# Performance work log

Measured on AMD Instinct MI355X. Metric: run time of the kernel, lower is better.

Reference implementation:

```python
import jax, jax.numpy as jnp
import numpy as np

D_MODEL = 1024
H = 16
D_K = D_MODEL // H
NEG = -1e9


def setup_inputs() -> dict:
    key = jax.random.key(0)
    ks = jax.random.split(key, 8)
    B, S = 4, 2048
    q = jax.random.normal(ks[0], (B, S, D_MODEL), dtype=jnp.float32)
    k = jax.random.normal(ks[1], (B, S, D_MODEL), dtype=jnp.float32)
    v = jax.random.normal(ks[2], (B, S, D_MODEL), dtype=jnp.float32)
    mask = jax.random.randint(ks[3], (B, S), 0, 2, dtype=jnp.int32)
    scale = 1.0 / np.sqrt(D_MODEL)
    Wq = jax.random.normal(ks[4], (D_MODEL, D_MODEL), dtype=jnp.float32) * scale
    Wk = jax.random.normal(ks[5], (D_MODEL, D_MODEL), dtype=jnp.float32) * scale
    Wv = jax.random.normal(ks[6], (D_MODEL, D_MODEL), dtype=jnp.float32) * scale
    Wo = jax.random.normal(ks[7], (D_MODEL, D_MODEL), dtype=jnp.float32) * scale
    return {"q": q, "k": k, "v": v, "mask": mask,
            "Wq": Wq, "Wk": Wk, "Wv": Wv, "Wo": Wo}


def _split_heads(x):
    # [B,S,d_model] -> [B,H,S,d_k]
    B, S, _ = x.shape
    return x.reshape(B, S, H, D_K).transpose(0, 2, 1, 3)


def reference(q, k, v, mask, Wq, Wk, Wv, Wo):
    # Linear projections (torch Linear: x @ W.T, no bias)
    query = _split_heads(jnp.einsum('bsd,ed->bse', q, Wq))
    key_ = _split_heads(jnp.einsum('bsd,ed->bse', k, Wk))
    value = _split_heads(jnp.einsum('bsd,ed->bse', v, Wv))
    # scaled dot-product attention, manual path
    scores = jnp.einsum('bhqd,bhkd->bhqk', query, key_) / jnp.sqrt(
        jnp.asarray(D_K, dtype=query.dtype))
    m = (mask == 0)[:, None, None, :]  # [B,1,1,S]
    scores = jnp.where(m, jnp.asarray(NEG, dtype=scores.dtype), scores)
    attn = jax.nn.softmax(scores, axis=-1)
    mh = jnp.einsum('bhqk,bhkd->bhqd', attn, value)
    # merge heads -> [B,S,d_model]
    B = mh.shape[0]
    mh = mh.transpose(0, 2, 1, 3).reshape(B, -1, D_MODEL)
    return jnp.einsum('bsd,ed->bse', mh, Wo)
```

## Files before the change

### kernel.cpp

```cpp
#include <hip/hip_runtime.h>
#include <math.h>

typedef __attribute__((ext_vector_type(4))) float f32x4;
typedef __attribute__((ext_vector_type(8))) __bf16 bf16x8;
typedef __attribute__((ext_vector_type(2))) __bf16 bf16x2;

#ifndef __has_builtin
#define __has_builtin(x) 0
#endif

#if __has_builtin(__builtin_amdgcn_exp2f)
#define EXP2F(x) __builtin_amdgcn_exp2f(x)
#else
#define EXP2F(x) exp2f(x)
#endif

__device__ __forceinline__ ushort f2bf(float f) {
  return (ushort)((__float_as_uint(f) + 0x8000u) >> 16);
}

__device__ __forceinline__ uint pack_bf16(float a, float b) {
#if __has_builtin(__builtin_amdgcn_cvt_pk_bf16_f32)
  bf16x2 p = __builtin_amdgcn_cvt_pk_bf16_f32(a, b);
  return __builtin_bit_cast(uint, p);
#elif __has_builtin(__builtin_amdgcn_perm)
  uint au = __float_as_uint(a) + 0x8000u;
  uint bu = __float_as_uint(b) + 0x8000u;
  return __builtin_amdgcn_perm(bu, au, 0x07060302u);
#else
  return (uint)f2bf(a) | ((uint)f2bf(b) << 16);
#endif
}

__device__ __forceinline__ void async_cp16(const void* g, void* l) {
  __builtin_amdgcn_global_load_lds(
      (const __attribute__((address_space(1))) void*)g,
      (__attribute__((address_space(3))) void*)l, 16, 0, 0);
}


__global__ __launch_bounds__(256) void prep_kernel(
    const float* __restrict__ q, const float* __restrict__ k, const float* __restrict__ v,
    const float* __restrict__ Wq, const float* __restrict__ Wk, const float* __restrict__ Wv,
    const float* __restrict__ Wo, const int* __restrict__ mask,
    ushort* qb, ushort* kb, ushort* vb,
    ushort* wqb, ushort* wkb, ushort* wvb, ushort* wob,
    ushort* biasbf) {
  int b = blockIdx.x;
  int tid = threadIdx.x;
  if (b < 4096) {
    int j = b >> 10;
    const float* in = j == 0 ? Wq : (j == 1 ? Wk : (j == 2 ? Wv : Wo));
    ushort* out = j == 0 ? wqb : (j == 1 ? wkb : (j == 2 ? wvb : wob));
    int i = (b & 1023) * 256 + tid;
    float4 f = ((const float4*)in)[i];
    uint2 o;
    o.x = pack_bf16(f.x, f.y);
    o.y = pack_bf16(f.z, f.w);
    ((uint2*)out)[i] = o;
  } else if (b < 28672) {
    int bb = b - 4096;
    int j = bb >> 13;
    const float* in = j == 0 ? q : (j == 1 ? k : v);
    ushort* out = j == 0 ? qb : (j == 1 ? kb : vb);
    int i = (bb & 8191) * 256 + tid;
    float4 f = ((const float4*)in)[i];
    uint2 o;
    o.x = pack_bf16(f.x, f.y);
    o.y = pack_bf16(f.z, f.w);
    ((uint2*)out)[i] = o;
  } else {
    int i = (b - 28672) * 256 + tid;
    biasbf[i] = mask[i] ? (ushort)0 : (ushort)0xCE6E;
  }
}


__device__ __forceinline__ void gemm_body(const ushort* __restrict__ A,
                                          const ushort* __restrict__ W,
                                          void* __restrict__ Cout, int mode,
                                          int bm, int bn) {
  constexpr int N = 1024, K = 1024;
  constexpr int NT = K / 64;
  __shared__ ushort As[2][128 * 64];
  __shared__ ushort Bs[2][64 * 64];
  const int tid = threadIdx.x;
  const int w = tid >> 6, lane = tid & 63;
  const int g = lane >> 4, cc = lane & 15;
  const int wm = (w >> 1) * 64, wn = (w & 1) * 32;

  f32x4 acc[4][2];
#pragma unroll
  for (int i = 0; i < 4; ++i)
#pragma unroll
    for (int j = 0; j < 2; ++j) acc[i][j] = (f32x4)0.0f;

  auto stage = [&](int k0, int buf) {
#pragma unroll
    for (int j = 0; j < 4; ++j) {
      int cbase = w * 256 + j * 64;
      int cid = cbase + lane;
      int row = cid & 127, kb = cid >> 7;
      async_cp16(A + (size_t)(bm + row) * K + k0 + kb * 8, &As[buf][cbase * 8]);
    }
#pragma unroll
    for (int j = 0; j < 2; ++j) {
      int cbase = w * 128 + j * 64;
      int cid = cbase + lane;
      int row = cid & 63, kb = cid >> 6;
      async_cp16(W + (size_t)(bn + row) * K + k0 + kb * 8, &Bs[buf][cbase * 8]);
    }
  };

  auto compute = [&](int cur) {
#pragma unroll
    for (int ks = 0; ks < 2; ++ks) {
      bf16x8 af[4], bfr[2];
#pragma unroll
      for (int mi = 0; mi < 4; ++mi)
        af[mi] = *(const bf16x8*)&As[cur][((ks * 4 + g) * 128 + wm + mi * 16 + cc) * 8];
#pragma unroll
      for (int ni = 0; ni < 2; ++ni)
        bfr[ni] = *(const bf16x8*)&Bs[cur][((ks * 4 + g) * 64 + wn + ni * 16 + cc) * 8];
      __builtin_amdgcn_s_setprio(1);
#pragma unroll
      for (int mi = 0; mi < 4; ++mi)
#pragma unroll
        for (int ni = 0; ni < 2; ++ni)
          acc[mi][ni] =
              __builtin_amdgcn_mfma_f32_16x16x32_bf16(af[mi], bfr[ni], acc[mi][ni], 0, 0, 0);
      __builtin_amdgcn_s_setprio(0);
    }
  };

  stage(0, 0);
  stage(64, 1);
  for (int it = 0; it < NT - 1; ++it) {
    const int cur = it & 1;
    asm volatile("s_waitcnt vmcnt(6)" ::: "memory");
    __builtin_amdgcn_s_barrier();
    __builtin_amdgcn_sched_barrier(0);
    compute(cur);
    __builtin_amdgcn_sched_barrier(0);
    __builtin_amdgcn_s_barrier();
    __builtin_amdgcn_sched_barrier(0);
    if (it < NT - 2) stage((it + 2) * 64, cur);
  }
  asm volatile("s_waitcnt vmcnt(0)" ::: "memory");
  __builtin_amdgcn_s_barrier();
  __builtin_amdgcn_sched_barrier(0);
  compute((NT - 1) & 1);

  const float qsc = 0.18033688011112042f;
#pragma unroll
  for (int mi = 0; mi < 4; ++mi) {
#pragma unroll
    for (int ni = 0; ni < 2; ++ni) {
#pragma unroll
      for (int r = 0; r < 4; ++r) {
        int row = bm + wm + mi * 16 + g * 4 + r;
        int col = bn + wn + ni * 16 + cc;
        float val = acc[mi][ni][r];
        if (mode == 0) {
          ((ushort*)Cout)[(size_t)row * N + col] = f2bf(val);
        } else if (mode == 1) {
          ((float*)Cout)[(size_t)row * N + col] = val;
        } else if (mode == 3) {
          ((ushort*)Cout)[(size_t)row * N + col] = f2bf(val * qsc);
        } else {
          int b = row >> 11, s = row & 2047;
          int h = col >> 6, d = col & 63;
          ((ushort*)Cout)[(size_t)((b * 16 + h) * 64 + d) * 2048 + s] = f2bf(val);
        }
      }
    }
  }
}

__device__ __forceinline__ void swz_tile(int* bm, int* bn) {
  int l = blockIdx.x + (blockIdx.y << 4);
  int t = ((l & 7) << 7) + (l >> 3);
  *bn = (t & 15) * 64;
  *bm = (t >> 4) * 128;
}

__global__ __launch_bounds__(256) void qkv_gemm_kernel(const ushort* qb, const ushort* kb,
                                                       const ushort* vb, const ushort* wq,
                                                       const ushort* wk, const ushort* wv,
                                                       ushort* Qp, ushort* Kp, ushort* Vt) {
  int z = blockIdx.z;
  const ushort* A = z == 0 ? qb : (z == 1 ? kb : vb);
  const ushort* W = z == 0 ? wq : (z == 1 ? wk : wv);
  void* C = z == 0 ? (void*)Qp : (z == 1 ? (void*)Kp : (void*)Vt);
  int bm, bn;
  swz_tile(&bm, &bn);
  gemm_body(A, W, C, z == 2 ? 2 : (z == 0 ? 3 : 0), bm, bn);
}

__global__ __launch_bounds__(256) void gemm_wo_kernel(const ushort* A, const ushort* W,
                                                      float* C) {
  int bm, bn;
  swz_tile(&bm, &bn);
  gemm_body(A, W, C, 1, bm, bn);
}

__global__ __launch_bounds__(256, 3) void attn_kernel(const ushort* __restrict__ Qp,
                                                      const ushort* __restrict__ Kp,
                                                      const ushort* __restrict__ Vt,
                                                      const ushort* __restrict__ biasbf,
                                                      ushort* __restrict__ mh) {
  constexpr int S = 2048, DM = 1024, DK = 64;
  constexpr int NKT = S / 64;
  __shared__ ushort k_lds[2][64 * 64];
  __shared__ ushort v_lds[2][64 * 64];
  __shared__ ushort pt_lds[4 * 2176];
  __shared__ ushort bias_lds[2048];

  const int bh = blockIdx.x;
  const int qt = blockIdx.y;
  const int b = bh >> 4, h = bh & 15;
  const int tid = threadIdx.x;
  const int w = tid >> 6, lane = tid & 63;
  const int g = lane >> 4, cc = lane & 15;
  ushort* ptw = &pt_lds[w * 2176];

  const int q0 = qt * 128 + w * 32;
  bf16x8 qf[2][2];
#pragma unroll
  for (int ni = 0; ni < 2; ++ni) {
    size_t row = (size_t)(b * S + q0 + ni * 16 + cc);
#pragma unroll
    for (int ks = 0; ks < 2; ++ks)
      qf[ks][ni] = *(const bf16x8*)&Qp[row * DM + h * DK + ks * 32 + g * 8];
  }

  {
    uint4 bvv = *(const uint4*)&biasbf[(size_t)b * S + tid * 8];
    *(uint4*)&bias_lds[tid * 8] = bvv;
  }
  asm volatile("s_waitcnt lgkmcnt(0)" ::: "memory");

  bf16x8 ones;
#pragma unroll
  for (int i = 0; i < 8; ++i) ones[i] = (__bf16)1.0f;

  f32x4 o_acc[4][2];
#pragma unroll
  for (int i = 0; i < 4; ++i)
#pragma unroll
    for (int j = 0; j < 2; ++j) o_acc[i][j] = (f32x4)0.0f;
  f32x4 l_acc[2] = {(f32x4)0.0f, (f32x4)0.0f};

  auto stage = [&](int kt, int buf) {
#pragma unroll
    for (int j = 0; j < 2; ++j) {
      int cb = j * 256 + w * 64;
      int cid = cb + lane;
      async_cp16(Kp + (size_t)(b * S + kt * 64 + (cid & 63)) * DM + h * DK + (cid >> 6) * 8,
                 &k_lds[buf][cb * 8]);
      async_cp16(Vt + (size_t)(bh * DK + (cid & 63)) * S + kt * 64 + (cid >> 6) * 8,
                 &v_lds[buf][cb * 8]);
    }
  };

  stage(0, 0);
  stage(1, 1);
  for (int kt = 0; kt < NKT; ++kt) {
    const int cur = kt & 1;
    if (kt < NKT - 1) {
      asm volatile("s_waitcnt vmcnt(4)" ::: "memory");
    } else {
      asm volatile("s_waitcnt vmcnt(0)" ::: "memory");
    }
    __builtin_amdgcn_s_barrier();
    __builtin_amdgcn_sched_barrier(0);

    f32x4 sacc[4][2];
#pragma unroll
    for (int mi = 0; mi < 4; ++mi)
#pragma unroll
      for (int ni = 0; ni < 2; ++ni) sacc[mi][ni] = (f32x4)0.0f;
    __builtin_amdgcn_s_setprio(1);
#pragma unroll
    for (int ks = 0; ks < 2; ++ks)
#pragma unroll
      for (int mi = 0; mi < 4; ++mi) {
        bf16x8 kf = *(const bf16x8*)&k_lds[cur][((ks * 4 + g) * 64 + mi * 16 + cc) * 8];
        sacc[mi][0] = __builtin_amdgcn_mfma_f32_16x16x32_bf16(kf, qf[ks][0], sacc[mi][0], 0, 0, 0);
        sacc[mi][1] = __builtin_amdgcn_mfma_f32_16x16x32_bf16(kf, qf[ks][1], sacc[mi][1], 0, 0, 0);
      }
    __builtin_amdgcn_s_setprio(0);

#pragma unroll
    for (int mi = 0; mi < 4; ++mi) {
      ushort4 bw = *(const ushort4*)&bias_lds[kt * 64 + mi * 16 + g * 4];
      float bvp[4];
      bvp[0] = __uint_as_float((uint)bw.x << 16);
      bvp[1] = __uint_as_float((uint)bw.y << 16);
      bvp[2] = __uint_as_float((uint)bw.z << 16);
      bvp[3] = __uint_as_float((uint)bw.w << 16);
#pragma unroll
      for (int ni = 0; ni < 2; ++ni) {
        float p0 = EXP2F(sacc[mi][ni][0] + bvp[0]);
        float p1 = EXP2F(sacc[mi][ni][1] + bvp[1]);
        float p2 = EXP2F(sacc[mi][ni][2] + bvp[2]);
        float p3 = EXP2F(sacc[mi][ni][3] + bvp[3]);
        uint2 pv;
        pv.x = pack_bf16(p0, p1);
        pv.y = pack_bf16(p2, p3);
        int base = ((mi * 2 + (g >> 1)) * 32 + ni * 16 + cc) * 8 + (g & 1) * 4;
        *(uint2*)&ptw[base] = pv;
      }
    }

    __builtin_amdgcn_s_setprio(1);
#pragma unroll
    for (int ks = 0; ks < 2; ++ks) {
      bf16x8 ptf[2];
#pragma unroll
      for (int ni = 0; ni < 2; ++ni)
        ptf[ni] = *(const bf16x8*)&ptw[((ks * 4 + g) * 32 + ni * 16 + cc) * 8];
      l_acc[0] = __builtin_amdgcn_mfma_f32_16x16x32_bf16(ones, ptf[0], l_acc[0], 0, 0, 0);
      l_acc[1] = __builtin_amdgcn_mfma_f32_16x16x32_bf16(ones, ptf[1], l_acc[1], 0, 0, 0);
#pragma unroll
      for (int md = 0; md < 4; ++md) {
        bf16x8 vf = *(const bf16x8*)&v_lds[cur][((ks * 4 + g) * 64 + md * 16 + cc) * 8];
        o_acc[md][0] = __builtin_amdgcn_mfma_f32_16x16x32_bf16(vf, ptf[0], o_acc[md][0], 0, 0, 0);
        o_acc[md][1] = __builtin_amdgcn_mfma_f32_16x16x32_bf16(vf, ptf[1], o_acc[md][1], 0, 0, 0);
      }
    }
    __builtin_amdgcn_s_setprio(0);

    if (kt < NKT - 1) {
      __builtin_amdgcn_sched_barrier(0);
      __builtin_amdgcn_s_barrier();
      __builtin_amdgcn_sched_barrier(0);
      if (kt < NKT - 2) stage(kt + 2, cur);
    }
  }

  float rl[2];
#pragma unroll
  for (int ni = 0; ni < 2; ++ni) rl[ni] = 1.0f / l_acc[ni][0];

#pragma unroll
  for (int md = 0; md < 4; ++md)
#pragma unroll
    for (int ni = 0; ni < 2; ++ni) {
      int ql = ni * 16 + cc;
      int dbase = md * 16 + g * 4;
      *(uint*)&ptw[ql * 68 + dbase] =
          pack_bf16(o_acc[md][ni][0] * rl[ni], o_acc[md][ni][1] * rl[ni]);
      *(uint*)&ptw[ql * 68 + dbase + 2] =
          pack_bf16(o_acc[md][ni][2] * rl[ni], o_acc[md][ni][3] * rl[ni]);
    }
#pragma unroll
  for (int pass = 0; pass < 4; ++pass) {
    int ql = pass * 8 + (lane >> 3);
    int dc = lane & 7;
    uint4 val = *(const uint4*)&ptw[ql * 68 + dc * 8];
    *(uint4*)&mh[(size_t)(b * S + q0 + ql) * DM + h * DK + dc * 8] = val;
  }
}


extern "C" void kernel_launch(void* const* d_in, const int* in_sizes, int n_in,
                              void* d_out, int out_size, void* d_ws, size_t ws_size,
                              hipStream_t stream) {
  const float* q = (const float*)d_in[0];
  const float* k = (const float*)d_in[1];
  const float* v = (const float*)d_in[2];
  const int* mask = (const int*)d_in[3];
  const float* Wq = (const float*)d_in[4];
  const float* Wk = (const float*)d_in[5];
  const float* Wv = (const float*)d_in[6];
  const float* Wo = (const float*)d_in[7];

  const size_t MB = 1 << 20;

  char* ws = (char*)d_ws;
  ushort* Qp = (ushort*)(ws);
  ushort* Kp = (ushort*)(ws + 16 * MB);
  ushort* Vt = (ushort*)(ws + 32 * MB);
  ushort* wqb = (ushort*)(ws + 48 * MB);
  ushort* wkb = wqb + (1 << 20);
  ushort* wvb = wkb + (1 << 20);
  ushort* wob = wvb + (1 << 20);
  ushort* biasbf = (ushort*)(ws + 56 * MB);
  ushort* vb = (ushort*)(ws + 57 * MB);
  ushort* mh = vb;
  ushort* qb = (ushort*)d_out;
  ushort* kb = qb + (size_t)8 * 1024 * 1024;

  prep_kernel<<<dim3(28704), dim3(256), 0, stream>>>(q, k, v, Wq, Wk, Wv, Wo, mask,
                                                     qb, kb, vb, wqb, wkb, wvb, wob, biasbf);
  qkv_gemm_kernel<<<dim3(16, 64, 3), dim3(256), 0, stream>>>(qb, kb, vb, wqb, wkb, wvb,
                                                             Qp, Kp, Vt);
  attn_kernel<<<dim3(64, 16), dim3(256), 0, stream>>>(Qp, Kp, Vt, biasbf, mh);
  gemm_wo_kernel<<<dim3(16, 64), dim3(256), 0, stream>>>(mh, wob, (float*)d_out);
}
```

Baseline: 461.9 us.

## Fuse fp32-to-bf16 activation conversion into QKV projection GEMM A-tile loads

Drops the separate pass that converted q, k, v from fp32 to bf16 into scratch buffers. The QKV GEMM now loads fp32 A tiles into registers, packs them to bf16, and writes them to LDS itself, with a register-prefetch pipeline. B tiles still use async global-to-LDS copies. This removes a full read/write round trip of about 100MB of activations, but the GEMM now reads twice as many A bytes from global memory per tile and adds conversion ALU work and register pressure inside the main loop.

```diff
diff --git a/kernel.cpp b/kernel.cpp
--- a/kernel.cpp
+++ b/kernel.cpp
@@ -40,10 +40,8 @@
 
 
 __global__ __launch_bounds__(256) void prep_kernel(
-    const float* __restrict__ q, const float* __restrict__ k, const float* __restrict__ v,
     const float* __restrict__ Wq, const float* __restrict__ Wk, const float* __restrict__ Wv,
     const float* __restrict__ Wo, const int* __restrict__ mask,
-    ushort* qb, ushort* kb, ushort* vb,
     ushort* wqb, ushort* wkb, ushort* wvb, ushort* wob,
     ushort* biasbf) {
   int b = blockIdx.x;
@@ -58,27 +56,139 @@
     o.x = pack_bf16(f.x, f.y);
     o.y = pack_bf16(f.z, f.w);
     ((uint2*)out)[i] = o;
-  } else if (b < 28672) {
-    int bb = b - 4096;
-    int j = bb >> 13;
-    const float* in = j == 0 ? q : (j == 1 ? k : v);
-    ushort* out = j == 0 ? qb : (j == 1 ? kb : vb);
-    int i = (bb & 8191) * 256 + tid;
-    float4 f = ((const float4*)in)[i];
-    uint2 o;
-    o.x = pack_bf16(f.x, f.y);
-    o.y = pack_bf16(f.z, f.w);
-    ((uint2*)out)[i] = o;
   } else {
-    int i = (b - 28672) * 256 + tid;
+    int i = (b - 4096) * 256 + tid;
     biasbf[i] = mask[i] ? (ushort)0 : (ushort)0xCE6E;
   }
 }
 
+
+__device__ __forceinline__ void gemm_fused_body(const float* __restrict__ A,
+                                                const ushort* __restrict__ W,
+                                                void* __restrict__ Cout, int mode,
+                                                int bm, int bn) {
+  constexpr int N = 1024, K = 1024;
+  constexpr int NT = K / 64;
+  __shared__ ushort As[2][128 * 64];
+  __shared__ ushort Bs[2][64 * 64];
+  const int tid = threadIdx.x;
+  const int w = tid >> 6, lane = tid & 63;
+  const int g = lane >> 4, cc = lane & 15;
+  const int wm = (w >> 1) * 64, wn = (w & 1) * 32;
+
+  const int arow = tid >> 1;
+  const int khalf = tid & 1;
+
+  f32x4 acc[4][2];
+#pragma unroll
+  for (int i = 0; i < 4; ++i)
+#pragma unroll
+    for (int j = 0; j < 2; ++j) acc[i][j] = (f32x4)0.0f;
+
+  f32x4 ar[8];
+
+  auto stageB = [&](int k0, int buf) {
+#pragma unroll
+    for (int j = 0; j < 2; ++j) {
+      int cbase = w * 128 + j * 64;
+      int cid = cbase + lane;
+      int row = cid & 63, kb = cid >> 6;
+      async_cp16(W + (size_t)(bn + row) * K + k0 + kb * 8, &Bs[buf][cbase * 8]);
+    }
+  };
+
+  auto loadA = [&](int k0) {
+#pragma unroll
+    for (int j = 0; j < 8; ++j)
+      ar[j] = *(const f32x4*)&A[(size_t)(bm + arow) * K + k0 + khalf * 32 + j * 4];
+  };
+
+  auto writeA = [&](int buf) {
+#pragma unroll
+    for (int p = 0; p < 4; ++p) {
+      int kb8 = khalf * 4 + p;
+      uint4 o;
+      o.x = pack_bf16(ar[2 * p][0], ar[2 * p][1]);
+      o.y = pack_bf16(ar[2 * p][2], ar[2 * p][3]);
+      o.z = pack_bf16(ar[2 * p + 1][0], ar[2 * p + 1][1]);
+      o.w = pack_bf16(ar[2 * p + 1][2], ar[2 * p + 1][3]);
+      *(uint4*)&As[buf][(kb8 * 128 + arow) * 8] = o;
+    }
+  };
+
+  auto compute = [&](int cur) {
+#pragma unroll
+    for (int ks = 0; ks < 2; ++ks) {
+      bf16x8 af[4], bfr[2];
+#pragma unroll
+      for (int mi = 0; mi < 4; ++mi)
+        af[mi] = *(const bf16x8*)&As[cur][((ks * 4 + g) * 128 + wm + mi * 16 + cc) * 8];
+#pragma unroll
+      for (int ni = 0; ni < 2; ++ni)
+        bfr[ni] = *(const bf16x8*)&Bs[cur][((ks * 4 + g) * 64 + wn + ni * 16 + cc) * 8];
+      __builtin_amdgcn_s_setprio(1);
+#pragma unroll
+      for (int mi = 0; mi < 4; ++mi)
+#pragma unroll
+        for (int ni = 0; ni < 2; ++ni)
+          acc[mi][ni] =
+              __builtin_amdgcn_mfma_f32_16x16x32_bf16(af[mi], bfr[ni], acc[mi][ni], 0, 0, 0);
+      __builtin_amdgcn_s_setprio(0);
+    }
+  };
+
+  stageB(0, 0);
+  loadA(0);
+  writeA(0);
+  stageB(64, 1);
+  loadA(64);
+  asm volatile("s_waitcnt lgkmcnt(0)" ::: "memory");
+
+  for (int t = 0; t < NT; ++t) {
+    const int cur = t & 1;
+    __builtin_amdgcn_s_barrier();
+    __builtin_amdgcn_sched_barrier(0);
+    compute(cur);
+    if (t + 1 < NT) {
+      writeA(cur ^ 1);
+      __builtin_amdgcn_sched_barrier(0);
+      asm volatile("s_waitcnt lgkmcnt(0)" ::: "memory");
+      __builtin_amdgcn_s_barrier();
+      __builtin_amdgcn_sched_barrier(0);
+      if (t + 2 < NT) {
+        stageB((t + 2) * 64, cur);
+        loadA((t + 2) * 64);
+      }
+    }
+  }
+
+  const float qsc = 0.18033688011112042f;
+#pragma unroll
+  for (int mi = 0; mi < 4; ++mi) {
+#pragma unroll
+    for (int ni = 0; ni < 2; ++ni) {
+#pragma unroll
+      for (int r = 0; r < 4; ++r) {
+        int row = bm + wm + mi * 16 + g * 4 + r;
+        int col = bn + wn + ni * 16 + cc;
+        float val = acc[mi][ni][r];
+        if (mode == 0) {
+          ((ushort*)Cout)[(size_t)row * N + col] = f2bf(val);
+        } else if (mode == 3) {
+          ((ushort*)Cout)[(size_t)row * N + col] = f2bf(val * qsc);
+        } else {
+          int b = row >> 11, s = row & 2047;
+          int h = col >> 6, d = col & 63;
+          ((ushort*)Cout)[(size_t)((b * 16 + h) * 64 + d) * 2048 + s] = f2bf(val);
+        }
+      }
+    }
+  }
+}
 
 __device__ __forceinline__ void gemm_body(const ushort* __restrict__ A,
                                           const ushort* __restrict__ W,
-                                          void* __restrict__ Cout, int mode,
+                                          float* __restrict__ Cout,
                                           int bm, int bn) {
   constexpr int N = 1024, K = 1024;
   constexpr int NT = K / 64;
@@ -151,30 +261,16 @@
   __builtin_amdgcn_sched_barrier(0);
   compute((NT - 1) & 1);
 
-  const float qsc = 0.18033688011112042f;
-#pragma unroll
-  for (int mi = 0; mi < 4; ++mi) {
-#pragma unroll
-    for (int ni = 0; ni < 2; ++ni) {
+#pragma unroll
+  for (int mi = 0; mi < 4; ++mi)
+#pragma unroll
+    for (int ni = 0; ni < 2; ++ni)
 #pragma unroll
       for (int r = 0; r < 4; ++r) {
         int row = bm + wm + mi * 16 + g * 4 + r;
         int col = bn + wn + ni * 16 + cc;
-        float val = acc[mi][ni][r];
-        if (mode == 0) {
-          ((ushort*)Cout)[(size_t)row * N + col] = f2bf(val);
-        } else if (mode == 1) {
-          ((float*)Cout)[(size_t)row * N + col] = val;
-        } else if (mode == 3) {
-          ((ushort*)Cout)[(size_t)row * N + col] = f2bf(val * qsc);
-        } else {
-          int b = row >> 11, s = row & 2047;
-          int h = col >> 6, d = col & 63;
-          ((ushort*)Cout)[(size_t)((b * 16 + h) * 64 + d) * 2048 + s] = f2bf(val);
-        }
-      }
-    }
-  }
+        Cout[(size_t)row * N + col] = acc[mi][ni][r];
+      }
 }
 
 __device__ __forceinline__ void swz_tile(int* bm, int* bn) {
@@ -184,24 +280,24 @@
   *bm = (t >> 4) * 128;
 }
 
-__global__ __launch_bounds__(256) void qkv_gemm_kernel(const ushort* qb, const ushort* kb,
-                                                       const ushort* vb, const ushort* wq,
+__global__ __launch_bounds__(256) void qkv_gemm_kernel(const float* q, const float* k,
+                                                       const float* v, const ushort* wq,
                                                        const ushort* wk, const ushort* wv,
                                                        ushort* Qp, ushort* Kp, ushort* Vt) {
   int z = blockIdx.z;
-  const ushort* A = z == 0 ? qb : (z == 1 ? kb : vb);
+  const float* A = z == 0 ? q : (z == 1 ? k : v);
   const ushort* W = z == 0 ? wq : (z == 1 ? wk : wv);
   void* C = z == 0 ? (void*)Qp : (z == 1 ? (void*)Kp : (void*)Vt);
   int bm, bn;
   swz_tile(&bm, &bn);
-  gemm_body(A, W, C, z == 2 ? 2 : (z == 0 ? 3 : 0), bm, bn);
+  gemm_fused_body(A, W, C, z == 2 ? 2 : (z == 0 ? 3 : 0), bm, bn);
 }
 
 __global__ __launch_bounds__(256) void gemm_wo_kernel(const ushort* A, const ushort* W,
                                                       float* C) {
   int bm, bn;
   swz_tile(&bm, &bn);
-  gemm_body(A, W, C, 1, bm, bn);
+  gemm_body(A, W, C, bm, bn);
 }
 
 __global__ __launch_bounds__(256, 3) void attn_kernel(const ushort* __restrict__ Qp,
@@ -387,14 +483,11 @@
   ushort* wvb = wkb + (1 << 20);
   ushort* wob = wvb + (1 << 20);
   ushort* biasbf = (ushort*)(ws + 56 * MB);
-  ushort* vb = (ushort*)(ws + 57 * MB);
-  ushort* mh = vb;
-  ushort* qb = (ushort*)d_out;
-  ushort* kb = qb + (size_t)8 * 1024 * 1024;
-
-  prep_kernel<<<dim3(28704), dim3(256), 0, stream>>>(q, k, v, Wq, Wk, Wv, Wo, mask,
-                                                     qb, kb, vb, wqb, wkb, wvb, wob, biasbf);
-  qkv_gemm_kernel<<<dim3(16, 64, 3), dim3(256), 0, stream>>>(qb, kb, vb, wqb, wkb, wvb,
+  ushort* mh = (ushort*)(ws + 57 * MB);
+
+  prep_kernel<<<dim3(4128), dim3(256), 0, stream>>>(Wq, Wk, Wv, Wo, mask,
+                                                    wqb, wkb, wvb, wob, biasbf);
+  qkv_gemm_kernel<<<dim3(16, 64, 3), dim3(256), 0, stream>>>(q, k, v, wqb, wkb, wvb,
                                                              Qp, Kp, Vt);
   attn_kernel<<<dim3(64, 16), dim3(256), 0, stream>>>(Qp, Kp, Vt, biasbf, mh);
   gemm_wo_kernel<<<dim3(16, 64), dim3(256), 0, stream>>>(mh, wob, (float*)d_out);
```

New measurement: 533.7 us. 15.5% more time.
